# Kernel tuning notes

Hardware: AMD Instinct MI355X
Metric: run time of the kernel (lower is better)

Reference implementation:

```python
import jax, jax.numpy as jnp
import numpy as np

# Standard SMPL kinematic tree (parent of joint i); root parent is -1.
PARENTS = [-1, 0, 0, 0, 1, 2, 3, 4, 5, 6, 7, 8, 9, 9, 9, 12, 13, 14, 16, 17, 18, 19, 20, 21]
NUM_JOINTS = 24
NUM_VERTICES = 6890
NUM_BETAS = 10
UNIT_FACTOR = 1.0  # unit='m'


def rotvec2mat(r):
    """Rodrigues formula. r: (..., 3) -> (..., 3, 3)."""
    theta = jnp.linalg.norm(r, axis=-1, keepdims=True)            # (..., 1)
    safe_theta = jnp.where(theta < 1e-8, 1.0, theta)
    axis = r / safe_theta
    x, y, z = axis[..., 0], axis[..., 1], axis[..., 2]
    zeros = jnp.zeros_like(x)
    K = jnp.stack([zeros, -z, y, z, zeros, -x, -y, x, zeros], axis=-1)
    K = K.reshape(r.shape[:-1] + (3, 3))
    t = theta[..., None]                                          # (..., 1, 1)
    eye = jnp.eye(3, dtype=r.dtype)
    return eye + jnp.sin(t) * K + (1.0 - jnp.cos(t)) * (K @ K)


def setup_inputs() -> dict:
    key = jax.random.key(0)
    ks = jax.random.split(key, 9)
    B = 1024
    pose_rotvecs = 0.3 * jax.random.normal(ks[0], (B, NUM_JOINTS, 3), jnp.float32)
    shape_betas = jax.random.normal(ks[1], (B, NUM_BETAS), jnp.float32)
    trans = jax.random.normal(ks[2], (B, 3), jnp.float32)
    v_template = jax.random.normal(ks[3], (NUM_VERTICES, 3), jnp.float32)
    shapedirs = 0.01 * jax.random.normal(ks[4], (NUM_VERTICES, 3, NUM_BETAS), jnp.float32)
    posedirs = 0.01 * jax.random.normal(ks[5], (NUM_VERTICES, 3, (NUM_JOINTS - 1) * 9), jnp.float32)
    J_template = jax.random.normal(ks[6], (NUM_JOINTS, 3), jnp.float32)
    J_shapedirs = 0.01 * jax.random.normal(ks[7], (NUM_JOINTS, 3, NUM_BETAS), jnp.float32)
    w = jax.random.uniform(ks[8], (NUM_VERTICES, NUM_JOINTS), jnp.float32)
    weights = w / jnp.sum(w, axis=-1, keepdims=True)  # skinning weights: rows sum to 1
    return dict(pose_rotvecs=pose_rotvecs, shape_betas=shape_betas, trans=trans,
                v_template=v_template, shapedirs=shapedirs, posedirs=posedirs,
                J_template=J_template, J_shapedirs=J_shapedirs, weights=weights)


def reference(pose_rotvecs, shape_betas, trans, v_template, shapedirs, posedirs,
              J_template, J_shapedirs, weights):
    B = pose_rotvecs.shape[0]
    parent_idx = jnp.asarray(PARENTS[1:], dtype=jnp.int32)  # (J-1,)

    # Parent-relative rotation matrices from rotation vectors.
    rel_rotmats = rotvec2mat(pose_rotvecs)                  # (B, J, 3, 3)

    # Kinematic chain: compose global rotations along the tree (J=24, fixed small loop).
    glob_list = [rel_rotmats[:, 0]]
    for i in range(1, NUM_JOINTS):
        glob_list.append(glob_list[PARENTS[i]] @ rel_rotmats[:, i])
    glob_rotmats = jnp.stack(glob_list, axis=1)             # (B, J, 3, 3)

    eye = jnp.broadcast_to(jnp.eye(3, dtype=rel_rotmats.dtype), (B, 1, 3, 3))
    parent_glob = jnp.concatenate([eye, glob_rotmats[:, parent_idx]], axis=1)  # (B, J, 3, 3)

    # Shaped joint locations (kid_factor = 0 default -> term vanishes).
    j = J_template + jnp.einsum('jcs,bs->bjc', J_shapedirs, shape_betas)       # (B, J, 3)
    j_parent = jnp.concatenate([jnp.zeros((B, 1, 3), j.dtype), j[:, parent_idx]], axis=1)
    bones = j - j_parent
    rotated_bones = jnp.einsum('bjCc,bjc->bjC', parent_glob, bones)

    pos_list = [j[:, 0]]
    for i in range(1, NUM_JOINTS):
        pos_list.append(pos_list[PARENTS[i]] + rotated_bones[:, i])
    glob_positions = jnp.stack(pos_list, axis=1)            # (B, J, 3)

    # Blendshapes: shape + pose correctives (kid term zero).
    pose_feature = rel_rotmats[:, 1:].reshape(B, (NUM_JOINTS - 1) * 9)
    v_posed = (v_template
               + jnp.einsum('vcp,bp->bvc', shapedirs, shape_betas)
               + jnp.einsum('vcp,bp->bvc', posedirs, pose_feature))            # (B, V, 3)

    # Linear blend skinning.
    translations = glob_positions - jnp.einsum('bjCc,bjc->bjC', glob_rotmats, j)  # (B, J, 3)
    blended_rot = jnp.einsum('vj,bjCc->bvCc', weights, glob_rotmats)              # (B, V, 3, 3)
    vertices = (jnp.einsum('bvCc,bvc->bvC', blended_rot, v_posed)
                + jnp.einsum('vj,bjc->bvc', weights, translations))               # (B, V, 3)

    joints = (glob_positions + trans[:, None]) * UNIT_FACTOR
    vertices = (vertices + trans[:, None]) * UNIT_FACTOR
    return joints, vertices, glob_rotmats
```

## Files before the change

### kernel.cpp

```cpp
#include <hip/hip_runtime.h>
#include <math.h>

#define NJ 24
#define NV 6890
#define NB 10
#define KREAL 217
#define KP 224
#define NVT 432

typedef __attribute__((ext_vector_type(8))) short bf16x8;
typedef __attribute__((ext_vector_type(8))) unsigned short u16x8;
typedef __attribute__((ext_vector_type(4))) float f32x4;

__device__ __forceinline__ unsigned short f2bf(float x) {
    unsigned int u = __float_as_uint(x);
    u += 0x7fffu + ((u >> 16) & 1u);
    return (unsigned short)(u >> 16);
}

__device__ __constant__ int c_path[NJ][9] = {
  {0,0,0,0,0,0,0,0,0},
  {0,1,0,0,0,0,0,0,0},
  {0,2,0,0,0,0,0,0,0},
  {0,3,0,0,0,0,0,0,0},
  {0,1,4,0,0,0,0,0,0},
  {0,2,5,0,0,0,0,0,0},
  {0,3,6,0,0,0,0,0,0},
  {0,1,4,7,0,0,0,0,0},
  {0,2,5,8,0,0,0,0,0},
  {0,3,6,9,0,0,0,0,0},
  {0,1,4,7,10,0,0,0,0},
  {0,2,5,8,11,0,0,0,0},
  {0,3,6,9,12,0,0,0,0},
  {0,3,6,9,13,0,0,0,0},
  {0,3,6,9,14,0,0,0,0},
  {0,3,6,9,12,15,0,0,0},
  {0,3,6,9,13,16,0,0,0},
  {0,3,6,9,14,17,0,0,0},
  {0,3,6,9,13,16,18,0,0},
  {0,3,6,9,14,17,19,0,0},
  {0,3,6,9,13,16,18,20,0},
  {0,3,6,9,14,17,19,21,0},
  {0,3,6,9,13,16,18,20,22},
  {0,3,6,9,14,17,19,21,23}};
__device__ __constant__ int c_plen[NJ] = {1,2,2,2,3,3,3,4,4,4,5,5,5,5,5,6,6,6,7,7,8,8,9,9};

__global__ __launch_bounds__(256)
void pack_kernel(const float* __restrict__ shapedirs, const float* __restrict__ posedirs,
                 unsigned short* __restrict__ dirsF)
{
    const int t = threadIdx.x;
    const int vt = t >> 6;
    const int lane = t & 63;
    const int kg = lane >> 4;
    const int vsub = lane & 15;
    const int vtg = blockIdx.x * 4 + vt;
    const int v = vtg * 16 + vsub;
    const int kt = blockIdx.y;

    #pragma unroll
    for (int c = 0; c < 3; ++c) {
        u16x8 o;
        #pragma unroll
        for (int i = 0; i < 8; ++i) {
            const int k = kt * 32 + kg * 8 + i;
            float val = 0.f;
            if (v < NV && k < KREAL)
                val = (k < NB) ? shapedirs[(size_t)v * 30 + c * NB + k]
                               : posedirs[(size_t)v * 621 + c * 207 + (k - NB)];
            o[i] = f2bf(val);
        }
        *(u16x8*)&dirsF[(((size_t)(kt * 3 + c) * NVT + vtg) * 64 + lane) * 8] = o;
    }
}

__global__ __launch_bounds__(64)
void prep_kernel(const float* __restrict__ pose, const float* __restrict__ betas,
                 const float* __restrict__ trans, const float* __restrict__ J_template,
                 const float* __restrict__ J_shapedirs,
                 float* __restrict__ joints_out, float* __restrict__ glob_out,
                 float* __restrict__ A_ws, unsigned short* __restrict__ coeffF, int B)
{
    const int b = blockIdx.x;
    const int t = threadIdx.x;
    __shared__ float s_beta[NB];
    __shared__ float s_rel[NJ][9];
    __shared__ float s_glob[NJ][9];
    __shared__ float s_j[NJ][3];

    if (t < NB) s_beta[t] = betas[b * NB + t];
    __syncthreads();

    if (t < NJ) {
        float rx = pose[b * 72 + t * 3 + 0];
        float ry = pose[b * 72 + t * 3 + 1];
        float rz = pose[b * 72 + t * 3 + 2];
        float th = sqrtf(rx * rx + ry * ry + rz * rz);
        float safe = (th < 1e-8f) ? 1.0f : th;
        float ax = rx / safe, ay = ry / safe, az = rz / safe;
        float s = sinf(th), c = cosf(th), omc = 1.0f - c;
        float aa = ax * ax + ay * ay + az * az;
        float K[9] = {0.f, -az, ay, az, 0.f, -ax, -ay, ax, 0.f};
        float A2[9] = {ax*ax - aa, ax*ay,      ax*az,
                       ay*ax,      ay*ay - aa, ay*az,
                       az*ax,      az*ay,      az*az - aa};
        #pragma unroll
        for (int r = 0; r < 3; ++r)
            #pragma unroll
            for (int cc = 0; cc < 3; ++cc)
                s_rel[t][r * 3 + cc] = ((r == cc) ? 1.0f : 0.0f)
                                     + s * K[r * 3 + cc] + omc * A2[r * 3 + cc];
        #pragma unroll
        for (int cc = 0; cc < 3; ++cc) {
            float acc = J_template[t * 3 + cc];
            #pragma unroll
            for (int q = 0; q < NB; ++q)
                acc = fmaf(J_shapedirs[(t * 3 + cc) * NB + q], s_beta[q], acc);
            s_j[t][cc] = acc;
        }
    }
    __syncthreads();

    if (t < NJ) {
        const int L = c_plen[t];
        float G[9];
        #pragma unroll
        for (int e = 0; e < 9; ++e) G[e] = s_rel[0][e];
        for (int sIdx = 1; sIdx < L; ++sIdx) {
            const int p = c_path[t][sIdx];
            float Tn[9];
            #pragma unroll
            for (int r = 0; r < 3; ++r)
                #pragma unroll
                for (int cc = 0; cc < 3; ++cc)
                    Tn[r * 3 + cc] = G[r * 3 + 0] * s_rel[p][0 * 3 + cc]
                                   + G[r * 3 + 1] * s_rel[p][1 * 3 + cc]
                                   + G[r * 3 + 2] * s_rel[p][2 * 3 + cc];
            #pragma unroll
            for (int e = 0; e < 9; ++e) G[e] = Tn[e];
        }
        #pragma unroll
        for (int e = 0; e < 9; ++e) s_glob[t][e] = G[e];
        #pragma unroll
        for (int e = 0; e < 9; ++e) glob_out[(size_t)b * 216 + t * 9 + e] = G[e];
    }
    __syncthreads();

    if (t < NJ) {
        const int L = c_plen[t];
        float px = s_j[0][0], py = s_j[0][1], pz = s_j[0][2];
        for (int sIdx = 1; sIdx < L; ++sIdx) {
            const int pk = c_path[t][sIdx];
            const int pp = c_path[t][sIdx - 1];
            float bx = s_j[pk][0] - s_j[pp][0];
            float by = s_j[pk][1] - s_j[pp][1];
            float bz = s_j[pk][2] - s_j[pp][2];
            px += s_glob[pp][0] * bx + s_glob[pp][1] * by + s_glob[pp][2] * bz;
            py += s_glob[pp][3] * bx + s_glob[pp][4] * by + s_glob[pp][5] * bz;
            pz += s_glob[pp][6] * bx + s_glob[pp][7] * by + s_glob[pp][8] * bz;
        }
        const float tx = trans[b * 3 + 0], ty = trans[b * 3 + 1], tz = trans[b * 3 + 2];
        joints_out[(size_t)b * 72 + t * 3 + 0] = px + tx;
        joints_out[(size_t)b * 72 + t * 3 + 1] = py + ty;
        joints_out[(size_t)b * 72 + t * 3 + 2] = pz + tz;
        const float jx = s_j[t][0], jy = s_j[t][1], jz = s_j[t][2];
        float T0 = px - (s_glob[t][0] * jx + s_glob[t][1] * jy + s_glob[t][2] * jz) + tx;
        float T1 = py - (s_glob[t][3] * jx + s_glob[t][4] * jy + s_glob[t][5] * jz) + ty;
        float T2 = pz - (s_glob[t][6] * jx + s_glob[t][7] * jy + s_glob[t][8] * jz) + tz;
        float* Ab = A_ws + ((size_t)b * NJ + t) * 12;
        Ab[0]  = s_glob[t][0]; Ab[1]  = s_glob[t][1]; Ab[2]  = s_glob[t][2]; Ab[3]  = T0;
        Ab[4]  = s_glob[t][3]; Ab[5]  = s_glob[t][4]; Ab[6]  = s_glob[t][5]; Ab[7]  = T1;
        Ab[8]  = s_glob[t][6]; Ab[9]  = s_glob[t][7]; Ab[10] = s_glob[t][8]; Ab[11] = T2;
    }
    __syncthreads();

    const int btg = b >> 4, bl = b & 15;
    for (int k = t; k < KP; k += 64) {
        float val;
        if (k < NB) val = s_beta[k];
        else if (k < KREAL) { const int p2 = k - NB; val = s_rel[1 + p2 / 9][p2 % 9]; }
        else val = 0.f;
        const int kt = k >> 5, kg = (k >> 3) & 3, i = k & 7;
        coeffF[(((size_t)kt * (B >> 4) + btg) * 64 + kg * 16 + bl) * 8 + i] = f2bf(val);
    }
}

__global__ __launch_bounds__(256)
void vert_kernel(const float4* __restrict__ dirsF, const float4* __restrict__ coeffF,
                 const float* __restrict__ A_ws, const float* __restrict__ v_template,
                 const float* __restrict__ weights, float* __restrict__ vert_out, int B)
{
    __shared__ float smem[13056];
    const int tid  = threadIdx.x;
    const int lane = tid & 63;
    const int w    = __builtin_amdgcn_readfirstlane(tid >> 6);
    const int vt   = w;
    const int vb4  = blockIdx.y * 4;
    const int bblk = blockIdx.x;
    const int nbt  = B >> 4;

    f32x4 acc[3][4];
    #pragma unroll
    for (int c = 0; c < 3; ++c)
        #pragma unroll
        for (int bt = 0; bt < 4; ++bt) {
            acc[c][bt][0] = 0.f; acc[c][bt][1] = 0.f; acc[c][bt][2] = 0.f; acc[c][bt][3] = 0.f;
        }

    for (int kt = 0; kt < 7; ++kt) {
        __syncthreads();
        #pragma unroll
        for (int s = 0; s < 3; ++s) {
            const int row = s * 256 + tid;
            const int ch = row >> 6, l2 = row & 63;
            *(float4*)&smem[row * 4] =
                dirsF[((size_t)(kt * 3 + (ch >> 2)) * NVT + vb4 + (ch & 3)) * 64 + l2];
        }
        __syncthreads();
        bf16x8 bq[4];
        #pragma unroll
        for (int bt = 0; bt < 4; ++bt)
            bq[bt] = *(const bf16x8*)&coeffF[((size_t)kt * nbt + bblk * 4 + bt) * 64 + lane];
        #pragma unroll
        for (int c = 0; c < 3; ++c) {
            const bf16x8 a = *(const bf16x8*)&smem[((c * 4 + vt) * 64 + lane) * 4];
            #pragma unroll
            for (int bt = 0; bt < 4; ++bt)
                acc[c][bt] = __builtin_amdgcn_mfma_f32_16x16x32_bf16(a, bq[bt], acc[c][bt], 0, 0, 0);
        }
    }

    const int vrow0 = (vb4 + vt) * 16 + ((lane >> 4) << 2);
    #pragma unroll
    for (int c = 0; c < 3; ++c) {
        float tv[4];
        #pragma unroll
        for (int r = 0; r < 4; ++r) {
            const int v = vrow0 + r;
            tv[r] = (v < NV) ? v_template[(size_t)v * 3 + c] : 0.f;
        }
        #pragma unroll
        for (int bt = 0; bt < 4; ++bt) {
            acc[c][bt][0] += tv[0]; acc[c][bt][1] += tv[1];
            acc[c][bt][2] += tv[2]; acc[c][bt][3] += tv[3];
        }
    }

    __syncthreads();
    #pragma unroll
    for (int c = 0; c < 3; ++c)
        #pragma unroll
        for (int bt = 0; bt < 4; ++bt) {
            const int bl = bt * 16 + (lane & 15);
            const int vl = vt * 16 + ((lane >> 4) << 2);
            #pragma unroll
            for (int r = 0; r < 4; ++r)
                smem[(c * 64 + bl) * 68 + vl + r] = acc[c][bt][r];
        }
    __syncthreads();

    const int v = vb4 * 16 + lane;
    if (v < NV) {
        float wj[NJ];
        const float4* wp = (const float4*)(weights + (size_t)v * NJ);
        #pragma unroll
        for (int q = 0; q < 6; ++q) {
            const float4 t4 = wp[q];
            wj[q * 4 + 0] = t4.x; wj[q * 4 + 1] = t4.y; wj[q * 4 + 2] = t4.z; wj[q * 4 + 3] = t4.w;
        }
        for (int i = 0; i < 16; ++i) {
            const int b = bblk * 64 + w * 16 + i;
            const float4* Ab = (const float4*)(A_ws + (size_t)b * (NJ * 12));
            float R0 = 0.f, R1 = 0.f, R2 = 0.f, R3 = 0.f, R4 = 0.f, R5 = 0.f,
                  R6 = 0.f, R7 = 0.f, R8 = 0.f, T0 = 0.f, T1 = 0.f, T2 = 0.f;
            #pragma unroll
            for (int jj = 0; jj < NJ; ++jj) {
                const float wv = wj[jj];
                const float4 a0 = Ab[jj * 3 + 0];
                const float4 a1 = Ab[jj * 3 + 1];
                const float4 a2 = Ab[jj * 3 + 2];
                R0 = fmaf(wv, a0.x, R0); R1 = fmaf(wv, a0.y, R1); R2 = fmaf(wv, a0.z, R2); T0 = fmaf(wv, a0.w, T0);
                R3 = fmaf(wv, a1.x, R3); R4 = fmaf(wv, a1.y, R4); R5 = fmaf(wv, a1.z, R5); T1 = fmaf(wv, a1.w, T1);
                R6 = fmaf(wv, a2.x, R6); R7 = fmaf(wv, a2.y, R7); R8 = fmaf(wv, a2.z, R8); T2 = fmaf(wv, a2.w, T2);
            }
            const int bl = w * 16 + i;
            const float vp0 = smem[(0 * 64 + bl) * 68 + lane];
            const float vp1 = smem[(1 * 64 + bl) * 68 + lane];
            const float vp2 = smem[(2 * 64 + bl) * 68 + lane];
            const float o0 = R0 * vp0 + R1 * vp1 + R2 * vp2 + T0;
            const float o1 = R3 * vp0 + R4 * vp1 + R5 * vp2 + T1;
            const float o2 = R6 * vp0 + R7 * vp1 + R8 * vp2 + T2;
            const size_t off = (size_t)b * (NV * 3) + (size_t)v * 3;
            vert_out[off + 0] = o0;
            vert_out[off + 1] = o1;
            vert_out[off + 2] = o2;
        }
    }
}

extern "C" void kernel_launch(void* const* d_in, const int* in_sizes, int n_in,
                              void* d_out, int out_size, void* d_ws, size_t ws_size,
                              hipStream_t stream) {
    const float* pose        = (const float*)d_in[0];
    const float* betas       = (const float*)d_in[1];
    const float* trans       = (const float*)d_in[2];
    const float* v_template  = (const float*)d_in[3];
    const float* shapedirs   = (const float*)d_in[4];
    const float* posedirs    = (const float*)d_in[5];
    const float* J_template  = (const float*)d_in[6];
    const float* J_shapedirs = (const float*)d_in[7];
    const float* weights     = (const float*)d_in[8];
    const int B = in_sizes[0] / 72;

    float* out = (float*)d_out;
    float* joints_out = out;
    float* vert_out   = out + (size_t)B * 72;
    float* glob_out   = out + (size_t)B * 72 + (size_t)B * NV * 3;

    char* ws = (char*)d_ws;
    const size_t a_bytes     = (size_t)B * 288 * 4;
    const size_t coeff_bytes = (size_t)7 * (B >> 4) * 64 * 16;
    float*          A_ws   = (float*)ws;
    unsigned short* coeffF = (unsigned short*)(ws + a_bytes);
    unsigned short* dirsF  = (unsigned short*)(ws + a_bytes + coeff_bytes);

    pack_kernel<<<dim3(108, 7), 256, 0, stream>>>(shapedirs, posedirs, dirsF);
    prep_kernel<<<dim3(B), 64, 0, stream>>>(pose, betas, trans, J_template, J_shapedirs,
                                            joints_out, glob_out, A_ws, coeffF, B);
    vert_kernel<<<dim3(B / 64, 108), 256, 0, stream>>>((const float4*)dirsF, (const float4*)coeffF,
                                                       A_ws, v_template, weights, vert_out, B);
}
```

Before: 247.4 us.

## Halve vert_kernel LDS staging and coalesce pack_kernel reads via shared tile

The vert_kernel epilogue now stages the blendshape accumulators through shared memory in two passes of 32 batches instead of one pass of 64. This roughly halves the LDS footprint, and the launch bound now requests 4 blocks per CU, aiming for higher occupancy. The cost is an extra barrier and a second staging round. pack_kernel now loads a 16-vertex tile of shapedirs/posedirs contiguously into LDS, then emits the packed bf16 layout from it, which is meant to give coalesced global reads. It runs with one block per vertex tile.

```diff
diff --git a/kernel.cpp b/kernel.cpp
--- a/kernel.cpp
+++ b/kernel.cpp
@@ -49,27 +49,32 @@
 void pack_kernel(const float* __restrict__ shapedirs, const float* __restrict__ posedirs,
                  unsigned short* __restrict__ dirsF)
 {
+    __shared__ unsigned short tile[16][3][240];
     const int t = threadIdx.x;
-    const int vt = t >> 6;
+    const int vtg = blockIdx.x;
+
+    for (int idx = t; idx < 16 * 3 * KP; idx += 256) {
+        const int v_l = idx / (3 * KP);
+        const int rem = idx - v_l * (3 * KP);
+        const int c = rem / KP;
+        const int k = rem - c * KP;
+        const int v = vtg * 16 + v_l;
+        float val = 0.f;
+        if (v < NV && k < KREAL)
+            val = (k < NB) ? shapedirs[(size_t)v * 30 + c * NB + k]
+                           : posedirs[(size_t)v * 621 + c * 207 + (k - NB)];
+        tile[v_l][c][k] = f2bf(val);
+    }
+    __syncthreads();
+
     const int lane = t & 63;
+    const int w = t >> 6;
     const int kg = lane >> 4;
     const int vsub = lane & 15;
-    const int vtg = blockIdx.x * 4 + vt;
-    const int v = vtg * 16 + vsub;
-    const int kt = blockIdx.y;
-
-    #pragma unroll
-    for (int c = 0; c < 3; ++c) {
-        u16x8 o;
-        #pragma unroll
-        for (int i = 0; i < 8; ++i) {
-            const int k = kt * 32 + kg * 8 + i;
-            float val = 0.f;
-            if (v < NV && k < KREAL)
-                val = (k < NB) ? shapedirs[(size_t)v * 30 + c * NB + k]
-                               : posedirs[(size_t)v * 621 + c * 207 + (k - NB)];
-            o[i] = f2bf(val);
-        }
+    for (int j2 = w; j2 < 21; j2 += 4) {
+        const int kt = j2 / 3;
+        const int c = j2 - kt * 3;
+        const u16x8 o = *(const u16x8*)&tile[vsub][c][kt * 32 + kg * 8];
         *(u16x8*)&dirsF[(((size_t)(kt * 3 + c) * NVT + vtg) * 64 + lane) * 8] = o;
     }
 }
@@ -185,12 +190,12 @@
     }
 }
 
-__global__ __launch_bounds__(256)
+__global__ __launch_bounds__(256, 4)
 void vert_kernel(const float4* __restrict__ dirsF, const float4* __restrict__ coeffF,
                  const float* __restrict__ A_ws, const float* __restrict__ v_template,
                  const float* __restrict__ weights, float* __restrict__ vert_out, int B)
 {
-    __shared__ float smem[13056];
+    __shared__ float smem[6336];
     const int tid  = threadIdx.x;
     const int lane = tid & 63;
     const int w    = __builtin_amdgcn_readfirstlane(tid >> 6);
@@ -246,54 +251,62 @@
         }
     }
 
-    __syncthreads();
-    #pragma unroll
-    for (int c = 0; c < 3; ++c)
-        #pragma unroll
-        for (int bt = 0; bt < 4; ++bt) {
-            const int bl = bt * 16 + (lane & 15);
-            const int vl = vt * 16 + ((lane >> 4) << 2);
-            #pragma unroll
-            for (int r = 0; r < 4; ++r)
-                smem[(c * 64 + bl) * 68 + vl + r] = acc[c][bt][r];
-        }
-    __syncthreads();
-
-    const int v = vb4 * 16 + lane;
-    if (v < NV) {
-        float wj[NJ];
-        const float4* wp = (const float4*)(weights + (size_t)v * NJ);
+    const int vglob = vb4 * 16 + lane;
+    float wj[NJ];
+    if (vglob < NV) {
+        const float4* wp = (const float4*)(weights + (size_t)vglob * NJ);
         #pragma unroll
         for (int q = 0; q < 6; ++q) {
             const float4 t4 = wp[q];
             wj[q * 4 + 0] = t4.x; wj[q * 4 + 1] = t4.y; wj[q * 4 + 2] = t4.z; wj[q * 4 + 3] = t4.w;
         }
-        for (int i = 0; i < 16; ++i) {
-            const int b = bblk * 64 + w * 16 + i;
-            const float4* Ab = (const float4*)(A_ws + (size_t)b * (NJ * 12));
-            float R0 = 0.f, R1 = 0.f, R2 = 0.f, R3 = 0.f, R4 = 0.f, R5 = 0.f,
-                  R6 = 0.f, R7 = 0.f, R8 = 0.f, T0 = 0.f, T1 = 0.f, T2 = 0.f;
-            #pragma unroll
-            for (int jj = 0; jj < NJ; ++jj) {
-                const float wv = wj[jj];
-                const float4 a0 = Ab[jj * 3 + 0];
-                const float4 a1 = Ab[jj * 3 + 1];
-                const float4 a2 = Ab[jj * 3 + 2];
-                R0 = fmaf(wv, a0.x, R0); R1 = fmaf(wv, a0.y, R1); R2 = fmaf(wv, a0.z, R2); T0 = fmaf(wv, a0.w, T0);
-                R3 = fmaf(wv, a1.x, R3); R4 = fmaf(wv, a1.y, R4); R5 = fmaf(wv, a1.z, R5); T1 = fmaf(wv, a1.w, T1);
-                R6 = fmaf(wv, a2.x, R6); R7 = fmaf(wv, a2.y, R7); R8 = fmaf(wv, a2.z, R8); T2 = fmaf(wv, a2.w, T2);
+    }
+
+    __syncthreads();
+
+    for (int p = 0; p < 2; ++p) {
+        if (p) __syncthreads();
+        #pragma unroll
+        for (int c = 0; c < 3; ++c)
+            #pragma unroll
+            for (int half = 0; half < 2; ++half) {
+                const int b32 = half * 16 + (lane & 15);
+                const int vl  = vt * 16 + ((lane >> 4) << 2);
+                const f32x4 av = acc[c][2 * p + half];
+                #pragma unroll
+                for (int r = 0; r < 4; ++r)
+                    smem[(c * 32 + b32) * 66 + vl + r] = av[r];
             }
-            const int bl = w * 16 + i;
-            const float vp0 = smem[(0 * 64 + bl) * 68 + lane];
-            const float vp1 = smem[(1 * 64 + bl) * 68 + lane];
-            const float vp2 = smem[(2 * 64 + bl) * 68 + lane];
-            const float o0 = R0 * vp0 + R1 * vp1 + R2 * vp2 + T0;
-            const float o1 = R3 * vp0 + R4 * vp1 + R5 * vp2 + T1;
-            const float o2 = R6 * vp0 + R7 * vp1 + R8 * vp2 + T2;
-            const size_t off = (size_t)b * (NV * 3) + (size_t)v * 3;
-            vert_out[off + 0] = o0;
-            vert_out[off + 1] = o1;
-            vert_out[off + 2] = o2;
+        __syncthreads();
+
+        if (vglob < NV) {
+            for (int i = 0; i < 8; ++i) {
+                const int b32 = w * 8 + i;
+                const int b = bblk * 64 + p * 32 + b32;
+                const float4* Ab = (const float4*)(A_ws + (size_t)b * (NJ * 12));
+                float R0 = 0.f, R1 = 0.f, R2 = 0.f, R3 = 0.f, R4 = 0.f, R5 = 0.f,
+                      R6 = 0.f, R7 = 0.f, R8 = 0.f, T0 = 0.f, T1 = 0.f, T2 = 0.f;
+                #pragma unroll
+                for (int jj = 0; jj < NJ; ++jj) {
+                    const float wv = wj[jj];
+                    const float4 a0 = Ab[jj * 3 + 0];
+                    const float4 a1 = Ab[jj * 3 + 1];
+                    const float4 a2 = Ab[jj * 3 + 2];
+                    R0 = fmaf(wv, a0.x, R0); R1 = fmaf(wv, a0.y, R1); R2 = fmaf(wv, a0.z, R2); T0 = fmaf(wv, a0.w, T0);
+                    R3 = fmaf(wv, a1.x, R3); R4 = fmaf(wv, a1.y, R4); R5 = fmaf(wv, a1.z, R5); T1 = fmaf(wv, a1.w, T1);
+                    R6 = fmaf(wv, a2.x, R6); R7 = fmaf(wv, a2.y, R7); R8 = fmaf(wv, a2.z, R8); T2 = fmaf(wv, a2.w, T2);
+                }
+                const float vp0 = smem[(0 * 32 + b32) * 66 + lane];
+                const float vp1 = smem[(1 * 32 + b32) * 66 + lane];
+                const float vp2 = smem[(2 * 32 + b32) * 66 + lane];
+                const float o0 = R0 * vp0 + R1 * vp1 + R2 * vp2 + T0;
+                const float o1 = R3 * vp0 + R4 * vp1 + R5 * vp2 + T1;
+                const float o2 = R6 * vp0 + R7 * vp1 + R8 * vp2 + T2;
+                const size_t off = (size_t)b * (NV * 3) + (size_t)vglob * 3;
+                vert_out[off + 0] = o0;
+                vert_out[off + 1] = o1;
+                vert_out[off + 2] = o2;
+            }
         }
     }
 }
@@ -324,7 +337,7 @@
     unsigned short* coeffF = (unsigned short*)(ws + a_bytes);
     unsigned short* dirsF  = (unsigned short*)(ws + a_bytes + coeff_bytes);
 
-    pack_kernel<<<dim3(108, 7), 256, 0, stream>>>(shapedirs, posedirs, dirsF);
+    pack_kernel<<<dim3(NVT), 256, 0, stream>>>(shapedirs, posedirs, dirsF);
     prep_kernel<<<dim3(B), 64, 0, stream>>>(pose, betas, trans, J_template, J_shapedirs,
                                             joints_out, glob_out, A_ws, coeffF, B);
     vert_kernel<<<dim3(B / 64, 108), 256, 0, stream>>>((const float4*)dirsF, (const float4*)coeffF,
```

New measurement: 221.4 us. 1.12x faster.
